# Performance work log

Hardware: AMD Instinct MI355X
Metric: run time of the kernel (lower is better)

Reference implementation:

```python
import jax, jax.numpy as jnp
import numpy as np

H = 1024   # hidden_size
I = 2048   # intermediate_size
E = 16     # num_experts
K = 2      # num_experts_per_tok
B, T = 2, 2048


def setup_inputs() -> dict:
    key = jax.random.key(0)
    k1, k2, k3, k4 = jax.random.split(key, 4)
    x = jax.random.normal(k1, (B, T, H), dtype=jnp.float32)
    # torch nn.Linear weight layout: [out_features, in_features]
    Wg = jax.random.normal(k2, (E, H), dtype=jnp.float32) * 0.02   # gate
    W1 = jax.random.normal(k3, (E, I, H), dtype=jnp.float32) * 0.02  # fc1 per expert
    W2 = jax.random.normal(k4, (E, H, I), dtype=jnp.float32) * 0.02  # fc2 per expert
    return {"x": x, "Wg": Wg, "W1": W1, "W2": W2}


def reference(x, Wg, W1, W2):
    Bq, Tq, Hq = x.shape
    nt = Bq * Tq
    x_flat = x.reshape(nt, Hq)                       # [nt, H]
    gate_logits = x_flat @ Wg.T                      # [nt, E]
    gate_probs = jax.nn.softmax(gate_logits, axis=-1)
    topk_vals, topk_idx = jax.lax.top_k(gate_probs, K)  # [nt, K]
    # dense combine weights: zero for unselected (token, expert) pairs
    rows = jnp.arange(nt)[:, None]                   # [nt, 1]
    cw = jnp.zeros((nt, E), dtype=x.dtype).at[rows, topk_idx].add(topk_vals)
    # per-expert dense SiLU-MLP; combine weight of 0 makes unselected
    # contributions exactly zero, matching the original gather/scatter math.
    y_flat = jnp.zeros_like(x_flat)
    for e in range(E):
        h = jax.nn.silu(x_flat @ W1[e].T)            # [nt, I]
        o = h @ W2[e].T                              # [nt, H]
        y_flat = y_flat + cw[:, e:e + 1] * o
    return y_flat.reshape(Bq, Tq, Hq)
```

## Files before the change

kernel.cpp:

```cpp
#include <hip/hip_runtime.h>
#include <hip/hip_bf16.h>

#define H_DIM 1024
#define I_DIM 2048
#define NEXP  16
#define NTOK  4096
#define BM 128
#define BN 128
#define BK 32
#define ABUF (BM*BK)
#define BBUF (BN*BK)
#define MAXS 10240
#define MAXRB (MAXS/BM)
#define NC1 (I_DIM/BN)
#define NC2 (H_DIM/BN)
#define PAIRS (NTOK*2)
#define SORT_T 256
#define PPT (PAIRS/SORT_T)

typedef __attribute__((ext_vector_type(8))) short short8;
typedef __attribute__((ext_vector_type(4))) short short4v;
typedef __attribute__((ext_vector_type(4))) float f32x4;

#define OFF_TOKE 256
#define OFF_TOKW (OFF_TOKE + PAIRS*4)
#define OFF_TOS  (OFF_TOKW + PAIRS*4)
#define OFF_WOS  (OFF_TOS + MAXS*4)
#define OFF_H    (OFF_WOS + MAXS*4)
#define OFF_XBF  (OFF_H + (size_t)MAXS*I_DIM*2)
#define OFF_WBF  (OFF_XBF + (size_t)NTOK*H_DIM*2)
#define NEED_XBF OFF_WBF
#define NEED_FULL (OFF_WBF + (size_t)NEXP*I_DIM*H_DIM*2)

#define GLDS16(gsrc, ldst) \
  __builtin_amdgcn_global_load_lds((const __attribute__((address_space(1))) void*)(gsrc), \
                                   (__attribute__((address_space(3))) void*)(ldst), 16, 0, 0)

__device__ inline short f2bf(float f) {
    union { float f; unsigned u; } v; v.f = f;
    unsigned u = v.u + 0x7FFFu + ((v.u >> 16) & 1u);
    return (short)(u >> 16);
}

__device__ inline short8 pack8(const float4 a, const float4 b) {
    return (short8){ f2bf(a.x), f2bf(a.y), f2bf(a.z), f2bf(a.w),
                     f2bf(b.x), f2bf(b.y), f2bf(b.z), f2bf(b.w) };
}

__device__ inline int xcd_swz(int bid, int nwg) {
    return (bid & 7) * (nwg >> 3) + (bid >> 3);
}

__global__ __launch_bounds__(256) void conv_kernel(
    const float* __restrict__ src, short* __restrict__ dst, int n8)
{
    int i = blockIdx.x * blockDim.x + threadIdx.x;
    const int stride = gridDim.x * blockDim.x;
    for (; i < n8; i += stride) {
        const float4 f0 = ((const float4*)src)[2*i];
        const float4 f1 = ((const float4*)src)[2*i+1];
        ((short8*)dst)[i] = pack8(f0, f1);
    }
}

template<bool WRITE_XBF>
__global__ __launch_bounds__(256) void gate_kernel(
    const float* __restrict__ x, const float* __restrict__ Wg,
    int* __restrict__ tokE, float* __restrict__ tokW, short* __restrict__ xbf)
{
    const int tok  = blockIdx.x * 4 + (threadIdx.x >> 6);
    const int lane = threadIdx.x & 63;
    const float4* xr = (const float4*)(x + (size_t)tok * H_DIM);

    float acc[NEXP];
#pragma unroll
    for (int e = 0; e < NEXP; e++) acc[e] = 0.f;
#pragma unroll
    for (int j = 0; j < H_DIM/4; j += 64) {
        const float4 xv = xr[j + lane];
        if constexpr (WRITE_XBF) {
            *(short4v*)(xbf + (size_t)tok * H_DIM + (j + lane) * 4) =
                (short4v){ f2bf(xv.x), f2bf(xv.y), f2bf(xv.z), f2bf(xv.w) };
        }
#pragma unroll
        for (int e = 0; e < NEXP; e++) {
            const float4 wv = ((const float4*)(Wg + e * H_DIM))[j + lane];
            acc[e] = fmaf(xv.x, wv.x, fmaf(xv.y, wv.y, fmaf(xv.z, wv.z, fmaf(xv.w, wv.w, acc[e]))));
        }
    }
#pragma unroll
    for (int off = 32; off; off >>= 1) {
#pragma unroll
        for (int e = 0; e < NEXP; e++) acc[e] += __shfl_xor(acc[e], off, 64);
    }
    if (lane == 0) {
        float m = acc[0];
#pragma unroll
        for (int e = 1; e < NEXP; e++) m = fmaxf(m, acc[e]);
        float p[NEXP]; float s = 0.f;
#pragma unroll
        for (int e = 0; e < NEXP; e++) { p[e] = __expf(acc[e] - m); s += p[e]; }
        int i1 = 0;
#pragma unroll
        for (int e = 1; e < NEXP; e++) if (acc[e] > acc[i1]) i1 = e;
        int i2 = -1;
#pragma unroll
        for (int e = 0; e < NEXP; e++) {
            if (e == i1) continue;
            if (i2 < 0 || acc[e] > acc[i2]) i2 = e;
        }
        const float inv = 1.f / s;
        tokE[tok*2+0] = i1; tokW[tok*2+0] = p[i1] * inv;
        tokE[tok*2+1] = i2; tokW[tok*2+1] = p[i2] * inv;
    }
}

__global__ __launch_bounds__(SORT_T) void sort_kernel(
    const int* __restrict__ tokE, const float* __restrict__ tokW,
    int* __restrict__ aoff, int* __restrict__ tok_of_slot, float* __restrict__ w_of_slot)
{
    __shared__ int hist[NEXP * SORT_T];
    __shared__ int tot[NEXP];
    __shared__ int aoff_l[NEXP + 1];

    const int tid = threadIdx.x;
    const int lane = tid & 63, wv = tid >> 6;

    int eloc[PPT];
#pragma unroll
    for (int i = 0; i < PPT; i++) eloc[i] = tokE[tid * PPT + i];

#pragma unroll
    for (int e = 0; e < NEXP; e++) hist[e * SORT_T + tid] = 0;
    __syncthreads();
#pragma unroll
    for (int i = 0; i < PPT; i++) hist[eloc[i] * SORT_T + tid]++;
    __syncthreads();

#pragma unroll
    for (int r = 0; r < 4; r++) {
        const int e = wv * 4 + r;
        const int base = e * SORT_T + lane * 4;
        int v0 = hist[base+0], v1 = hist[base+1], v2 = hist[base+2], v3 = hist[base+3];
        const int s = v0 + v1 + v2 + v3;
        int incl = s;
#pragma unroll
        for (int off = 1; off < 64; off <<= 1) {
            const int t = __shfl_up(incl, off, 64);
            if (lane >= off) incl += t;
        }
        int run = incl - s;
        hist[base+0] = run; run += v0;
        hist[base+1] = run; run += v1;
        hist[base+2] = run; run += v2;
        hist[base+3] = run;
        if (lane == 63) tot[e] = incl;
    }
    __syncthreads();

    if (tid == 0) {
        int acc = 0;
#pragma unroll
        for (int e = 0; e < NEXP; e++) {
            aoff_l[e] = acc; aoff[e] = acc;
            acc += ((tot[e] + BM - 1) / BM) * BM;
        }
        aoff_l[NEXP] = acc; aoff[NEXP] = acc;
    }
    __syncthreads();

#pragma unroll
    for (int i = 0; i < PPT; i++) {
        const int p = tid * PPT + i;
        const int e = eloc[i];
        const int idx = hist[e * SORT_T + tid]++;
        const int slot = aoff_l[e] + idx;
        tok_of_slot[slot] = p >> 1;
        w_of_slot[slot] = tokW[p];
    }
}

__global__ __launch_bounds__(256) void fc1_bf16_kernel(
    const short* __restrict__ xbf, const short* __restrict__ w1bf,
    const int* __restrict__ aoff, const int* __restrict__ tok_of_slot,
    short* __restrict__ h)
{
    const int wg = xcd_swz(blockIdx.x, NC1 * MAXRB);
    const int colb = wg % NC1, rowb = wg / NC1;
    const int total = aoff[NEXP];
    const int row0 = rowb * BM;
    if (row0 >= total) return;
    int e = 0;
    while (aoff[e+1] <= row0) e++;
    const int col0 = colb * BN;

    __shared__ short As[ABUF];
    __shared__ short Bs[BBUF];

    const int tid = threadIdx.x, wid = tid>>6, lane = tid&63;
    const int wr = wid>>1, wc = wid&1;
    const int srow = wid*32 + (lane>>2);
    const int skc  = (lane&3)*8;

    int t0 = tok_of_slot[row0 + srow];      if (t0 < 0) t0 = 0;
    int t1 = tok_of_slot[row0 + srow + 16]; if (t1 < 0) t1 = 0;

    const short* sa0 = xbf + (size_t)t0 * H_DIM + skc;
    const short* sa1 = xbf + (size_t)t1 * H_DIM + skc;
    const short* wb  = w1bf + (size_t)e * I_DIM * H_DIM;
    const short* sb0 = wb + (size_t)(col0 + srow)      * H_DIM + skc;
    const short* sb1 = wb + (size_t)(col0 + srow + 16) * H_DIM + skc;

    short* la0 = &As[(wid*2+0)*512];
    short* la1 = &As[(wid*2+1)*512];
    short* lb0 = &Bs[(wid*2+0)*512];
    short* lb1 = &Bs[(wid*2+1)*512];

    const int frow = lane & 15, fko = (lane>>4)*8;

    f32x4 acc[4][4];
#pragma unroll
    for (int m=0;m<4;m++)
#pragma unroll
        for (int n=0;n<4;n++) acc[m][n] = (f32x4){0.f,0.f,0.f,0.f};

    for (int k0 = 0; k0 < H_DIM; k0 += BK) {
        GLDS16(sa0 + k0, la0);
        GLDS16(sa1 + k0, la1);
        GLDS16(sb0 + k0, lb0);
        GLDS16(sb1 + k0, lb1);
        __syncthreads();

        short8 af[4], bfr[4];
#pragma unroll
        for (int m=0;m<4;m++) af[m]  = *(const short8*)&As[(wr*64 + m*16 + frow)*32 + fko];
#pragma unroll
        for (int n=0;n<4;n++) bfr[n] = *(const short8*)&Bs[(wc*64 + n*16 + frow)*32 + fko];
#pragma unroll
        for (int m=0;m<4;m++)
#pragma unroll
            for (int n=0;n<4;n++)
                acc[m][n] = __builtin_amdgcn_mfma_f32_16x16x32_bf16(af[m], bfr[n], acc[m][n], 0, 0, 0);
        __syncthreads();
    }

    const int mr0 = row0 + wr*64 + (lane>>4)*4;
    const int nc0 = col0 + wc*64 + (lane&15);
#pragma unroll
    for (int m=0;m<4;m++)
#pragma unroll
        for (int n=0;n<4;n++)
#pragma unroll
            for (int r=0;r<4;r++) {
                const float v = acc[m][n][r];
                const float sv = v / (1.f + __expf(-v));
                h[(size_t)(mr0 + m*16 + r) * I_DIM + nc0 + n*16] = f2bf(sv);
            }
}

template<int AMODE>
__global__ __launch_bounds__(256) void fc1_kernel_t(
    const void* __restrict__ xsrc, const float* __restrict__ W1,
    const int* __restrict__ aoff, const int* __restrict__ tok_of_slot,
    short* __restrict__ h)
{
    const int wg = xcd_swz(blockIdx.x, NC1 * MAXRB);
    const int colb = wg % NC1, rowb = wg / NC1;
    const int total = aoff[NEXP];
    const int row0 = rowb * BM;
    if (row0 >= total) return;
    int e = 0;
    while (aoff[e+1] <= row0) e++;
    const int col0 = colb * BN;

    __shared__ short As[2*ABUF];
    __shared__ short Bs[2*BBUF];

    const int tid = threadIdx.x, wid = tid>>6, lane = tid&63;
    const int wr = wid>>1, wc = wid&1;
    const int srow = wid*32 + (lane>>2);
    const int skc  = (lane&3)*8;

    int t0 = tok_of_slot[row0 + srow];      if (t0 < 0) t0 = 0;
    int t1 = tok_of_slot[row0 + srow + 16]; if (t1 < 0) t1 = 0;

    const float* wf0 = W1 + (size_t)e * I_DIM * H_DIM + (size_t)(col0 + srow)      * H_DIM + skc;
    const float* wf1 = W1 + (size_t)e * I_DIM * H_DIM + (size_t)(col0 + srow + 16) * H_DIM + skc;

    const short *sa0=nullptr,*sa1=nullptr;
    const float *fa0=nullptr,*fa1=nullptr;
    if constexpr (AMODE == 0) {
        const short* xb = (const short*)xsrc;
        sa0 = xb + (size_t)t0 * H_DIM + skc;
        sa1 = xb + (size_t)t1 * H_DIM + skc;
    } else {
        const float* xf = (const float*)xsrc;
        fa0 = xf + (size_t)t0 * H_DIM + skc;
        fa1 = xf + (size_t)t1 * H_DIM + skc;
    }
    short* la0 = &As[(wid*2+0)*512];
    short* la1 = &As[(wid*2+1)*512];

    const int frow = lane & 15, fko = (lane>>4)*8;

    f32x4 acc[4][4];
#pragma unroll
    for (int m=0;m<4;m++)
#pragma unroll
        for (int n=0;n<4;n++) acc[m][n] = (f32x4){0.f,0.f,0.f,0.f};

    float4 b00 = *(const float4*)(wf0), b01 = *(const float4*)(wf0+4);
    float4 b10 = *(const float4*)(wf1), b11 = *(const float4*)(wf1+4);
    float4 a00, a01, a10, a11;
    if constexpr (AMODE == 0) {
        GLDS16(sa0, la0);
        GLDS16(sa1, la1);
    } else {
        a00 = *(const float4*)(fa0); a01 = *(const float4*)(fa0+4);
        a10 = *(const float4*)(fa1); a11 = *(const float4*)(fa1+4);
        *(short8*)&As[srow*32 + skc]      = pack8(a00, a01);
        *(short8*)&As[(srow+16)*32 + skc] = pack8(a10, a11);
    }
    *(short8*)&Bs[srow*32 + skc]      = pack8(b00, b01);
    *(short8*)&Bs[(srow+16)*32 + skc] = pack8(b10, b11);
    __syncthreads();

    const int NT = H_DIM / BK;
    int cur = 0;
    for (int t = 0; t < NT; ++t) {
        const int kn = (t+1)*BK;
        const bool more = (t+1 < NT);
        if (more) {
            if constexpr (AMODE == 0) {
                GLDS16(sa0 + kn, la0 + (cur^1)*ABUF);
                GLDS16(sa1 + kn, la1 + (cur^1)*ABUF);
            } else {
                a00 = *(const float4*)(fa0+kn); a01 = *(const float4*)(fa0+kn+4);
                a10 = *(const float4*)(fa1+kn); a11 = *(const float4*)(fa1+kn+4);
            }
            b00 = *(const float4*)(wf0+kn); b01 = *(const float4*)(wf0+kn+4);
            b10 = *(const float4*)(wf1+kn); b11 = *(const float4*)(wf1+kn+4);
        }

        short8 af[4], bfr[4];
#pragma unroll
        for (int m=0;m<4;m++) af[m]  = *(const short8*)&As[cur*ABUF + (wr*64 + m*16 + frow)*32 + fko];
#pragma unroll
        for (int n=0;n<4;n++) bfr[n] = *(const short8*)&Bs[cur*BBUF + (wc*64 + n*16 + frow)*32 + fko];
#pragma unroll
        for (int m=0;m<4;m++)
#pragma unroll
            for (int n=0;n<4;n++)
                acc[m][n] = __builtin_amdgcn_mfma_f32_16x16x32_bf16(af[m], bfr[n], acc[m][n], 0, 0, 0);

        if (more) {
            if constexpr (AMODE == 1) {
                *(short8*)&As[(cur^1)*ABUF + srow*32 + skc]      = pack8(a00, a01);
                *(short8*)&As[(cur^1)*ABUF + (srow+16)*32 + skc] = pack8(a10, a11);
            }
            *(short8*)&Bs[(cur^1)*BBUF + srow*32 + skc]      = pack8(b00, b01);
            *(short8*)&Bs[(cur^1)*BBUF + (srow+16)*32 + skc] = pack8(b10, b11);
        }
        __syncthreads();
        cur ^= 1;
    }

    const int mr0 = row0 + wr*64 + (lane>>4)*4;
    const int nc0 = col0 + wc*64 + (lane&15);
#pragma unroll
    for (int m=0;m<4;m++)
#pragma unroll
        for (int n=0;n<4;n++)
#pragma unroll
            for (int r=0;r<4;r++) {
                const float v = acc[m][n][r];
                const float sv = v / (1.f + __expf(-v));
                h[(size_t)(mr0 + m*16 + r) * I_DIM + nc0 + n*16] = f2bf(sv);
            }
}

template<int MODE>
__global__ __launch_bounds__(256) void fc2_kernel_t(
    const short* __restrict__ h, const void* __restrict__ w2src,
    const int* __restrict__ aoff, const int* __restrict__ tok_of_slot,
    const float* __restrict__ w_of_slot, float* __restrict__ y)
{
    const int wg = xcd_swz(blockIdx.x, NC2 * MAXRB);
    const int colb = wg % NC2, rowb = wg / NC2;
    const int total = aoff[NEXP];
    const int row0 = rowb * BM;
    if (row0 >= total) return;
    int e = 0;
    while (aoff[e+1] <= row0) e++;
    const int col0 = colb * BN;

    __shared__ short As[ABUF];
    __shared__ short Bs[BBUF];

    const int tid = threadIdx.x, wid = tid>>6, lane = tid&63;
    const int wr = wid>>1, wc = wid&1;
    const int srow = wid*32 + (lane>>2);
    const int skc  = (lane&3)*8;

    const short* sa0 = h + (size_t)(row0 + srow)      * I_DIM + skc;
    const short* sa1 = h + (size_t)(row0 + srow + 16) * I_DIM + skc;

    const short *sb0=nullptr,*sb1=nullptr;
    const float *fb0=nullptr,*fb1=nullptr;
    if constexpr (MODE == 0) {
        const short* wb = (const short*)w2src + (size_t)e * H_DIM * I_DIM;
        sb0 = wb + (size_t)(col0 + srow)      * I_DIM + skc;
        sb1 = wb + (size_t)(col0 + srow + 16) * I_DIM + skc;
    } else {
        const float* wf = (const float*)w2src + (size_t)e * H_DIM * I_DIM;
        fb0 = wf + (size_t)(col0 + srow)      * I_DIM + skc;
        fb1 = wf + (size_t)(col0 + srow + 16) * I_DIM + skc;
    }
    short* la0 = &As[(wid*2+0)*512];
    short* la1 = &As[(wid*2+1)*512];
    short* lb0 = &Bs[(wid*2+0)*512];
    short* lb1 = &Bs[(wid*2+1)*512];

    const int frow = lane & 15, fko = (lane>>4)*8;

    f32x4 acc[4][4];
#pragma unroll
    for (int m=0;m<4;m++)
#pragma unroll
        for (int n=0;n<4;n++) acc[m][n] = (f32x4){0.f,0.f,0.f,0.f};

    for (int k0 = 0; k0 < I_DIM; k0 += BK) {
        GLDS16(sa0 + k0, la0);
        GLDS16(sa1 + k0, la1);
        if constexpr (MODE == 0) {
            GLDS16(sb0 + k0, lb0);
            GLDS16(sb1 + k0, lb1);
        } else {
            const float4 b00 = *(const float4*)(fb0 + k0), b01 = *(const float4*)(fb0 + k0 + 4);
            const float4 b10 = *(const float4*)(fb1 + k0), b11 = *(const float4*)(fb1 + k0 + 4);
            *(short8*)&Bs[srow*32 + skc]      = pack8(b00, b01);
            *(short8*)&Bs[(srow+16)*32 + skc] = pack8(b10, b11);
        }
        __syncthreads();

        short8 af[4], bfr[4];
#pragma unroll
        for (int m=0;m<4;m++) af[m]  = *(const short8*)&As[(wr*64 + m*16 + frow)*32 + fko];
#pragma unroll
        for (int n=0;n<4;n++) bfr[n] = *(const short8*)&Bs[(wc*64 + n*16 + frow)*32 + fko];
#pragma unroll
        for (int m=0;m<4;m++)
#pragma unroll
            for (int n=0;n<4;n++)
                acc[m][n] = __builtin_amdgcn_mfma_f32_16x16x32_bf16(af[m], bfr[n], acc[m][n], 0, 0, 0);
        __syncthreads();
    }

    const int mr0 = row0 + wr*64 + (lane>>4)*4;
    const int nc0 = col0 + wc*64 + (lane&15);
#pragma unroll
    for (int m=0;m<4;m++)
#pragma unroll
        for (int r=0;r<4;r++) {
            const int slot = mr0 + m*16 + r;
            const int tok = tok_of_slot[slot];
            if (tok < 0) continue;
            const float w = w_of_slot[slot];
#pragma unroll
            for (int n=0;n<4;n++)
                atomicAdd(&y[(size_t)tok * H_DIM + nc0 + n*16], w * acc[m][n][r]);
        }
}

extern "C" void kernel_launch(void* const* d_in, const int* in_sizes, int n_in,
                              void* d_out, int out_size, void* d_ws, size_t ws_size,
                              hipStream_t stream) {
    const float* x  = (const float*)d_in[0];
    const float* Wg = (const float*)d_in[1];
    const float* W1 = (const float*)d_in[2];
    const float* W2 = (const float*)d_in[3];
    float* y = (float*)d_out;

    char* ws = (char*)d_ws;
    int*   aoff        = (int*)  (ws + 128);
    int*   tokE        = (int*)  (ws + OFF_TOKE);
    float* tokW        = (float*)(ws + OFF_TOKW);
    int*   tok_of_slot = (int*)  (ws + OFF_TOS);
    float* w_of_slot   = (float*)(ws + OFF_WOS);
    short* h           = (short*)(ws + OFF_H);
    short* xbf         = (short*)(ws + OFF_XBF);
    short* wbf         = (short*)(ws + OFF_WBF);

    const bool full   = (ws_size >= NEED_FULL);
    const bool hasXbf = (ws_size >= NEED_XBF);

    hipMemsetAsync(tok_of_slot, 0xFF, MAXS*4, stream);
    hipMemsetAsync(y, 0, (size_t)out_size * 4, stream);

    if (full) {
        gate_kernel<true><<<NTOK/4, 256, 0, stream>>>(x, Wg, tokE, tokW, xbf);
        sort_kernel<<<1, SORT_T, 0, stream>>>(tokE, tokW, aoff, tok_of_slot, w_of_slot);
        conv_kernel<<<2048, 256, 0, stream>>>(W1, wbf, NEXP*I_DIM*H_DIM/8);
        fc1_bf16_kernel<<<NC1*MAXRB, 256, 0, stream>>>(xbf, wbf, aoff, tok_of_slot, h);
        conv_kernel<<<2048, 256, 0, stream>>>(W2, wbf, NEXP*H_DIM*I_DIM/8);
        fc2_kernel_t<0><<<NC2*MAXRB, 256, 0, stream>>>(h, wbf, aoff, tok_of_slot, w_of_slot, y);
    } else if (hasXbf) {
        gate_kernel<true><<<NTOK/4, 256, 0, stream>>>(x, Wg, tokE, tokW, xbf);
        sort_kernel<<<1, SORT_T, 0, stream>>>(tokE, tokW, aoff, tok_of_slot, w_of_slot);
        fc1_kernel_t<0><<<NC1*MAXRB, 256, 0, stream>>>(xbf, W1, aoff, tok_of_slot, h);
        fc2_kernel_t<1><<<NC2*MAXRB, 256, 0, stream>>>(h, W2, aoff, tok_of_slot, w_of_slot, y);
    } else {
        gate_kernel<false><<<NTOK/4, 256, 0, stream>>>(x, Wg, tokE, tokW, nullptr);
        sort_kernel<<<1, SORT_T, 0, stream>>>(tokE, tokW, aoff, tok_of_slot, w_of_slot);
        fc1_kernel_t<1><<<NC1*MAXRB, 256, 0, stream>>>(x, W1, aoff, tok_of_slot, h);
        fc2_kernel_t<1><<<NC2*MAXRB, 256, 0, stream>>>(h, W2, aoff, tok_of_slot, w_of_slot, y);
    }
}
```

Measured before the change: 260.3 us.

## Use 256x256 tiles with 512-thread blocks for bf16 expert GEMMs

```diff
diff --git a/kernel.cpp b/kernel.cpp
--- a/kernel.cpp
+++ b/kernel.cpp
@@ -5,15 +5,23 @@
 #define I_DIM 2048
 #define NEXP  16
 #define NTOK  4096
+#define BK 32
+
 #define BM 128
 #define BN 128
-#define BK 32
 #define ABUF (BM*BK)
 #define BBUF (BN*BK)
-#define MAXS 10240
-#define MAXRB (MAXS/BM)
+
+#define BM2 256
+#define BN2 256
+#define MAXS 12288
+#define MAXRB1 (MAXS/BM)
+#define MAXRB2 (MAXS/BM2)
 #define NC1 (I_DIM/BN)
 #define NC2 (H_DIM/BN)
+#define NC1B (I_DIM/BN2)
+#define NC2B (H_DIM/BN2)
+
 #define PAIRS (NTOK*2)
 #define SORT_T 256
 #define PPT (PAIRS/SORT_T)
@@ -115,6 +123,7 @@
     }
 }
 
+template<int ALIGN>
 __global__ __launch_bounds__(SORT_T) void sort_kernel(
     const int* __restrict__ tokE, const float* __restrict__ tokW,
     int* __restrict__ aoff, int* __restrict__ tok_of_slot, float* __restrict__ w_of_slot)
@@ -163,7 +172,7 @@
 #pragma unroll
         for (int e = 0; e < NEXP; e++) {
             aoff_l[e] = acc; aoff[e] = acc;
-            acc += ((tot[e] + BM - 1) / BM) * BM;
+            acc += ((tot[e] + ALIGN - 1) / ALIGN) * ALIGN;
         }
         aoff_l[NEXP] = acc; aoff[NEXP] = acc;
     }
@@ -180,47 +189,47 @@
     }
 }
 
-__global__ __launch_bounds__(256) void fc1_bf16_kernel(
+__global__ __launch_bounds__(512) void fc1_big_kernel(
     const short* __restrict__ xbf, const short* __restrict__ w1bf,
     const int* __restrict__ aoff, const int* __restrict__ tok_of_slot,
     short* __restrict__ h)
 {
-    const int wg = xcd_swz(blockIdx.x, NC1 * MAXRB);
-    const int colb = wg % NC1, rowb = wg / NC1;
+    const int wg = xcd_swz(blockIdx.x, NC1B * MAXRB2);
+    const int colb = wg % NC1B, rowb = wg / NC1B;
     const int total = aoff[NEXP];
-    const int row0 = rowb * BM;
+    const int row0 = rowb * BM2;
     if (row0 >= total) return;
     int e = 0;
     while (aoff[e+1] <= row0) e++;
-    const int col0 = colb * BN;
-
-    __shared__ short As[ABUF];
-    __shared__ short Bs[BBUF];
+    const int col0 = colb * BN2;
+
+    __shared__ short As[BM2*BK];
+    __shared__ short Bs[BN2*BK];
 
     const int tid = threadIdx.x, wid = tid>>6, lane = tid&63;
-    const int wr = wid>>1, wc = wid&1;
-    const int srow = wid*32 + (lane>>2);
-    const int skc  = (lane&3)*8;
-
-    int t0 = tok_of_slot[row0 + srow];      if (t0 < 0) t0 = 0;
-    int t1 = tok_of_slot[row0 + srow + 16]; if (t1 < 0) t1 = 0;
+    const int wr = wid>>2, wc = wid&3;
+    const int srow = tid>>2;
+    const int skc  = (tid&3)*8;
+
+    int t0 = tok_of_slot[row0 + srow];       if (t0 < 0) t0 = 0;
+    int t1 = tok_of_slot[row0 + srow + 128]; if (t1 < 0) t1 = 0;
 
     const short* sa0 = xbf + (size_t)t0 * H_DIM + skc;
     const short* sa1 = xbf + (size_t)t1 * H_DIM + skc;
     const short* wb  = w1bf + (size_t)e * I_DIM * H_DIM;
-    const short* sb0 = wb + (size_t)(col0 + srow)      * H_DIM + skc;
-    const short* sb1 = wb + (size_t)(col0 + srow + 16) * H_DIM + skc;
-
-    short* la0 = &As[(wid*2+0)*512];
-    short* la1 = &As[(wid*2+1)*512];
-    short* lb0 = &Bs[(wid*2+0)*512];
-    short* lb1 = &Bs[(wid*2+1)*512];
+    const short* sb0 = wb + (size_t)(col0 + srow)       * H_DIM + skc;
+    const short* sb1 = wb + (size_t)(col0 + srow + 128) * H_DIM + skc;
+
+    short* la0 = &As[wid*512];
+    short* la1 = &As[4096 + wid*512];
+    short* lb0 = &Bs[wid*512];
+    short* lb1 = &Bs[4096 + wid*512];
 
     const int frow = lane & 15, fko = (lane>>4)*8;
 
-    f32x4 acc[4][4];
-#pragma unroll
-    for (int m=0;m<4;m++)
+    f32x4 acc[8][4];
+#pragma unroll
+    for (int m=0;m<8;m++)
 #pragma unroll
         for (int n=0;n<4;n++) acc[m][n] = (f32x4){0.f,0.f,0.f,0.f};
 
@@ -231,23 +240,23 @@
         GLDS16(sb1 + k0, lb1);
         __syncthreads();
 
-        short8 af[4], bfr[4];
-#pragma unroll
-        for (int m=0;m<4;m++) af[m]  = *(const short8*)&As[(wr*64 + m*16 + frow)*32 + fko];
+        short8 bfr[4];
 #pragma unroll
         for (int n=0;n<4;n++) bfr[n] = *(const short8*)&Bs[(wc*64 + n*16 + frow)*32 + fko];
 #pragma unroll
-        for (int m=0;m<4;m++)
+        for (int m=0;m<8;m++) {
+            const short8 af = *(const short8*)&As[(wr*128 + m*16 + frow)*32 + fko];
 #pragma unroll
             for (int n=0;n<4;n++)
-                acc[m][n] = __builtin_amdgcn_mfma_f32_16x16x32_bf16(af[m], bfr[n], acc[m][n], 0, 0, 0);
-        __syncthreads();
-    }
-
-    const int mr0 = row0 + wr*64 + (lane>>4)*4;
+                acc[m][n] = __builtin_amdgcn_mfma_f32_16x16x32_bf16(af, bfr[n], acc[m][n], 0, 0, 0);
+        }
+        __syncthreads();
+    }
+
+    const int mr0 = row0 + wr*128 + (lane>>4)*4;
     const int nc0 = col0 + wc*64 + (lane&15);
 #pragma unroll
-    for (int m=0;m<4;m++)
+    for (int m=0;m<8;m++)
 #pragma unroll
         for (int n=0;n<4;n++)
 #pragma unroll
@@ -258,13 +267,90 @@
             }
 }
 
+__global__ __launch_bounds__(512) void fc2_big_kernel(
+    const short* __restrict__ h, const short* __restrict__ w2bf,
+    const int* __restrict__ aoff, const int* __restrict__ tok_of_slot,
+    const float* __restrict__ w_of_slot, float* __restrict__ y)
+{
+    const int wg = xcd_swz(blockIdx.x, NC2B * MAXRB2);
+    const int colb = wg % NC2B, rowb = wg / NC2B;
+    const int total = aoff[NEXP];
+    const int row0 = rowb * BM2;
+    if (row0 >= total) return;
+    int e = 0;
+    while (aoff[e+1] <= row0) e++;
+    const int col0 = colb * BN2;
+
+    __shared__ short As[BM2*BK];
+    __shared__ short Bs[BN2*BK];
+
+    const int tid = threadIdx.x, wid = tid>>6, lane = tid&63;
+    const int wr = wid>>2, wc = wid&3;
+    const int srow = tid>>2;
+    const int skc  = (tid&3)*8;
+
+    const short* sa0 = h + (size_t)(row0 + srow)       * I_DIM + skc;
+    const short* sa1 = h + (size_t)(row0 + srow + 128) * I_DIM + skc;
+    const short* wb  = w2bf + (size_t)e * H_DIM * I_DIM;
+    const short* sb0 = wb + (size_t)(col0 + srow)       * I_DIM + skc;
+    const short* sb1 = wb + (size_t)(col0 + srow + 128) * I_DIM + skc;
+
+    short* la0 = &As[wid*512];
+    short* la1 = &As[4096 + wid*512];
+    short* lb0 = &Bs[wid*512];
+    short* lb1 = &Bs[4096 + wid*512];
+
+    const int frow = lane & 15, fko = (lane>>4)*8;
+
+    f32x4 acc[8][4];
+#pragma unroll
+    for (int m=0;m<8;m++)
+#pragma unroll
+        for (int n=0;n<4;n++) acc[m][n] = (f32x4){0.f,0.f,0.f,0.f};
+
+    for (int k0 = 0; k0 < I_DIM; k0 += BK) {
+        GLDS16(sa0 + k0, la0);
+        GLDS16(sa1 + k0, la1);
+        GLDS16(sb0 + k0, lb0);
+        GLDS16(sb1 + k0, lb1);
+        __syncthreads();
+
+        short8 bfr[4];
+#pragma unroll
+        for (int n=0;n<4;n++) bfr[n] = *(const short8*)&Bs[(wc*64 + n*16 + frow)*32 + fko];
+#pragma unroll
+        for (int m=0;m<8;m++) {
+            const short8 af = *(const short8*)&As[(wr*128 + m*16 + frow)*32 + fko];
+#pragma unroll
+            for (int n=0;n<4;n++)
+                acc[m][n] = __builtin_amdgcn_mfma_f32_16x16x32_bf16(af, bfr[n], acc[m][n], 0, 0, 0);
+        }
+        __syncthreads();
+    }
+
+    const int mr0 = row0 + wr*128 + (lane>>4)*4;
+    const int nc0 = col0 + wc*64 + (lane&15);
+#pragma unroll
+    for (int m=0;m<8;m++)
+#pragma unroll
+        for (int r=0;r<4;r++) {
+            const int slot = mr0 + m*16 + r;
+            const int tok = tok_of_slot[slot];
+            if (tok < 0) continue;
+            const float w = w_of_slot[slot];
+#pragma unroll
+            for (int n=0;n<4;n++)
+                atomicAdd(&y[(size_t)tok * H_DIM + nc0 + n*16], w * acc[m][n][r]);
+        }
+}
+
 template<int AMODE>
 __global__ __launch_bounds__(256) void fc1_kernel_t(
     const void* __restrict__ xsrc, const float* __restrict__ W1,
     const int* __restrict__ aoff, const int* __restrict__ tok_of_slot,
     short* __restrict__ h)
 {
-    const int wg = xcd_swz(blockIdx.x, NC1 * MAXRB);
+    const int wg = xcd_swz(blockIdx.x, NC1 * MAXRB1);
     const int colb = wg % NC1, rowb = wg / NC1;
     const int total = aoff[NEXP];
     const int row0 = rowb * BM;
@@ -379,13 +465,12 @@
             }
 }
 
-template<int MODE>
-__global__ __launch_bounds__(256) void fc2_kernel_t(
-    const short* __restrict__ h, const void* __restrict__ w2src,
+__global__ __launch_bounds__(256) void fc2_kernel_f(
+    const short* __restrict__ h, const float* __restrict__ W2,
     const int* __restrict__ aoff, const int* __restrict__ tok_of_slot,
     const float* __restrict__ w_of_slot, float* __restrict__ y)
 {
-    const int wg = xcd_swz(blockIdx.x, NC2 * MAXRB);
+    const int wg = xcd_swz(blockIdx.x, NC2 * MAXRB1);
     const int colb = wg % NC2, rowb = wg / NC2;
     const int total = aoff[NEXP];
     const int row0 = rowb * BM;
@@ -404,22 +489,11 @@
 
     const short* sa0 = h + (size_t)(row0 + srow)      * I_DIM + skc;
     const short* sa1 = h + (size_t)(row0 + srow + 16) * I_DIM + skc;
-
-    const short *sb0=nullptr,*sb1=nullptr;
-    const float *fb0=nullptr,*fb1=nullptr;
-    if constexpr (MODE == 0) {
-        const short* wb = (const short*)w2src + (size_t)e * H_DIM * I_DIM;
-        sb0 = wb + (size_t)(col0 + srow)      * I_DIM + skc;
-        sb1 = wb + (size_t)(col0 + srow + 16) * I_DIM + skc;
-    } else {
-        const float* wf = (const float*)w2src + (size_t)e * H_DIM * I_DIM;
-        fb0 = wf + (size_t)(col0 + srow)      * I_DIM + skc;
-        fb1 = wf + (size_t)(col0 + srow + 16) * I_DIM + skc;
-    }
+    const float* fb0 = W2 + (size_t)e * H_DIM * I_DIM + (size_t)(col0 + srow)      * I_DIM + skc;
+    const float* fb1 = W2 + (size_t)e * H_DIM * I_DIM + (size_t)(col0 + srow + 16) * I_DIM + skc;
+
     short* la0 = &As[(wid*2+0)*512];
     short* la1 = &As[(wid*2+1)*512];
-    short* lb0 = &Bs[(wid*2+0)*512];
-    short* lb1 = &Bs[(wid*2+1)*512];
 
     const int frow = lane & 15, fko = (lane>>4)*8;
 
@@ -432,15 +506,10 @@
     for (int k0 = 0; k0 < I_DIM; k0 += BK) {
         GLDS16(sa0 + k0, la0);
         GLDS16(sa1 + k0, la1);
-        if constexpr (MODE == 0) {
-            GLDS16(sb0 + k0, lb0);
-            GLDS16(sb1 + k0, lb1);
-        } else {
-            const float4 b00 = *(const float4*)(fb0 + k0), b01 = *(const float4*)(fb0 + k0 + 4);
-            const float4 b10 = *(const float4*)(fb1 + k0), b11 = *(const float4*)(fb1 + k0 + 4);
-            *(short8*)&Bs[srow*32 + skc]      = pack8(b00, b01);
-            *(short8*)&Bs[(srow+16)*32 + skc] = pack8(b10, b11);
-        }
+        const float4 b00 = *(const float4*)(fb0 + k0), b01 = *(const float4*)(fb0 + k0 + 4);
+        const float4 b10 = *(const float4*)(fb1 + k0), b11 = *(const float4*)(fb1 + k0 + 4);
+        *(short8*)&Bs[srow*32 + skc]      = pack8(b00, b01);
+        *(short8*)&Bs[(srow+16)*32 + skc] = pack8(b10, b11);
         __syncthreads();
 
         short8 af[4], bfr[4];
@@ -499,20 +568,20 @@
 
     if (full) {
         gate_kernel<true><<<NTOK/4, 256, 0, stream>>>(x, Wg, tokE, tokW, xbf);
-        sort_kernel<<<1, SORT_T, 0, stream>>>(tokE, tokW, aoff, tok_of_slot, w_of_slot);
+        sort_kernel<BM2><<<1, SORT_T, 0, stream>>>(tokE, tokW, aoff, tok_of_slot, w_of_slot);
         conv_kernel<<<2048, 256, 0, stream>>>(W1, wbf, NEXP*I_DIM*H_DIM/8);
-        fc1_bf16_kernel<<<NC1*MAXRB, 256, 0, stream>>>(xbf, wbf, aoff, tok_of_slot, h);
+        fc1_big_kernel<<<NC1B*MAXRB2, 512, 0, stream>>>(xbf, wbf, aoff, tok_of_slot, h);
         conv_kernel<<<2048, 256, 0, stream>>>(W2, wbf, NEXP*H_DIM*I_DIM/8);
-        fc2_kernel_t<0><<<NC2*MAXRB, 256, 0, stream>>>(h, wbf, aoff, tok_of_slot, w_of_slot, y);
+        fc2_big_kernel<<<NC2B*MAXRB2, 512, 0, stream>>>(h, wbf, aoff, tok_of_slot, w_of_slot, y);
     } else if (hasXbf) {
         gate_kernel<true><<<NTOK/4, 256, 0, stream>>>(x, Wg, tokE, tokW, xbf);
-        sort_kernel<<<1, SORT_T, 0, stream>>>(tokE, tokW, aoff, tok_of_slot, w_of_slot);
-        fc1_kernel_t<0><<<NC1*MAXRB, 256, 0, stream>>>(xbf, W1, aoff, tok_of_slot, h);
-        fc2_kernel_t<1><<<NC2*MAXRB, 256, 0, stream>>>(h, W2, aoff, tok_of_slot, w_of_slot, y);
+        sort_kernel<BM><<<1, SORT_T, 0, stream>>>(tokE, tokW, aoff, tok_of_slot, w_of_slot);
+        fc1_kernel_t<0><<<NC1*MAXRB1, 256, 0, stream>>>(xbf, W1, aoff, tok_of_slot, h);
+        fc2_kernel_f<<<NC2*MAXRB1, 256, 0, stream>>>(h, W2, aoff, tok_of_slot, w_of_slot, y);
     } else {
         gate_kernel<false><<<NTOK/4, 256, 0, stream>>>(x, Wg, tokE, tokW, nullptr);
-        sort_kernel<<<1, SORT_T, 0, stream>>>(tokE, tokW, aoff, tok_of_slot, w_of_slot);
-        fc1_kernel_t<1><<<NC1*MAXRB, 256, 0, stream>>>(x, W1, aoff, tok_of_slot, h);
-        fc2_kernel_t<1><<<NC2*MAXRB, 256, 0, stream>>>(h, W2, aoff, tok_of_slot, w_of_slot, y);
-    }
-}
+        sort_kernel<BM><<<1, SORT_T, 0, stream>>>(tokE, tokW, aoff, tok_of_slot, w_of_slot);
+        fc1_kernel_t<1><<<NC1*MAXRB1, 256, 0, stream>>>(x, W1, aoff, tok_of_slot, h);
+        fc2_kernel_f<<<NC2*MAXRB1, 256, 0, stream>>>(h, W2, aoff, tok_of_slot, w_of_slot, y);
+    }
+}
```

Result: slower. 326.8 us (+25.5%).
